# Kernel optimization log

Hardware: AMD Instinct MI355X
Metric: run time of the kernel (lower is better)

## Reference

```python
import jax, jax.numpy as jnp
import numpy as np

B, C, H, W = 32, 256, 64, 64
GROUPS = 32                      # factor
CG = C // GROUPS                 # channels per group = 8
EPS = 1e-5                       # GroupNorm eps (torch default)


def setup_inputs() -> dict:
    key = jax.random.key(0)
    ks = jax.random.split(key, 5)
    x = jax.random.normal(ks[0], (B, C, H, W), dtype=jnp.float32)
    # conv1x1: [out=CG, in=CG] (kernel 1x1 collapsed to a matrix)
    w1 = jax.random.normal(ks[1], (CG, CG), dtype=jnp.float32) * (1.0 / np.sqrt(CG))
    b1 = jax.random.normal(ks[2], (CG,), dtype=jnp.float32) * 0.01
    # conv3x3: OIHW [CG, CG, 3, 3]
    w3 = jax.random.normal(ks[3], (CG, CG, 3, 3), dtype=jnp.float32) * (1.0 / np.sqrt(9 * CG))
    b3 = jax.random.normal(ks[4], (CG,), dtype=jnp.float32) * 0.01
    # GroupNorm(num_groups=CG, num_channels=CG) affine params
    gn_w = jnp.ones((CG,), dtype=jnp.float32)
    gn_b = jnp.zeros((CG,), dtype=jnp.float32)
    return {"x": x, "w1": w1, "b1": b1, "w3": w3, "b3": b3, "gn_w": gn_w, "gn_b": gn_b}


def reference(x, w1, b1, w3, b3, gn_w, gn_b):
    b, c, h, w = x.shape
    cg = c // GROUPS
    bg = b * GROUPS
    gx = x.reshape(bg, cg, h, w)

    # coordinate pooling
    x_h = gx.mean(axis=3, keepdims=True)                       # [bg, cg, h, 1]
    x_w = gx.mean(axis=2, keepdims=True).transpose(0, 1, 3, 2)  # [bg, cg, w, 1]

    # conv1x1 over concatenated coordinates (pure channel mix)
    hw = jnp.einsum('oc,bclk->bolk', w1, jnp.concatenate([x_h, x_w], axis=2))
    hw = hw + b1[None, :, None, None]                           # [bg, cg, h+w, 1]
    xh = hw[:, :, :h, :]                                        # [bg, cg, h, 1]
    xw = hw[:, :, h:, :].transpose(0, 1, 3, 2)                  # [bg, cg, 1, w]

    gated = gx * jax.nn.sigmoid(xh) * jax.nn.sigmoid(xw)        # [bg, cg, h, w]

    # GroupNorm(num_groups=cg, num_channels=cg): per-(sample,channel) spatial norm
    mu = gated.mean(axis=(2, 3), keepdims=True)
    var = gated.var(axis=(2, 3), keepdims=True)                 # biased var, matches torch
    x1 = (gated - mu) * jax.lax.rsqrt(var + EPS)
    x1 = x1 * gn_w[None, :, None, None] + gn_b[None, :, None, None]

    # conv3x3, padding=1 (SAME)
    x2 = jax.lax.conv_general_dilated(
        gx, w3, window_strides=(1, 1), padding='SAME',
        dimension_numbers=('NCHW', 'OIHW', 'NCHW'))
    x2 = x2 + b3[None, :, None, None]                           # [bg, cg, h, w]

    # cross channel-attention: softmax over pooled channels, matmul with flattened maps
    x11 = jax.nn.softmax(x1.mean(axis=(2, 3)), axis=-1)         # [bg, cg]
    x21 = jax.nn.softmax(x2.mean(axis=(2, 3)), axis=-1)         # [bg, cg]
    x12 = x2.reshape(bg, cg, h * w)
    x22 = x1.reshape(bg, cg, h * w)
    y = jnp.einsum('bc,bcl->bl', x11, x12) + jnp.einsum('bc,bcl->bl', x21, x22)

    weights = jax.nn.sigmoid(y).reshape(bg, 1, h, w)
    return (gx * weights).reshape(b, c, h, w)
```

## Files before the change

kernel.cpp:

```cpp
#include <hip/hip_runtime.h>

#define EPS 1e-5f
#define PSTRIDE 1120

__launch_bounds__(256, 4)
__global__ void k1_stats(const float* __restrict__ x,
                         const float* __restrict__ w1,
                         const float* __restrict__ b1,
                         const float* __restrict__ w3,
                         const float* __restrict__ b3,
                         const float* __restrict__ gn_w,
                         const float* __restrict__ gn_b,
                         float* __restrict__ params)
{
  __shared__ float rs[512];
  __shared__ float cs[512];
  __shared__ float sh[512];
  __shared__ float sw[512];
  __shared__ float colpart[2048];
  __shared__ float wavepart[64];
  __shared__ float Ssum[8], mu_s[8], rstd_s[8], m2[8], x11[8], alpha[8];
  __shared__ float corners[32];
  __shared__ float kc_s;

  const int t    = threadIdx.x;
  const int g    = blockIdx.x;
  const int q    = t & 15;
  const int rg   = t >> 4;
  const int wv   = t >> 6;
  const int lane = t & 63;
  const float*  xg  = x + (size_t)g * 32768;
  const float4* xg4 = (const float4*)xg;

  float4 cacc[8];
#pragma unroll
  for (int c = 0; c < 8; ++c) cacc[c] = make_float4(0.f, 0.f, 0.f, 0.f);
#pragma unroll
  for (int c = 0; c < 8; ++c) {
#pragma unroll
    for (int k = 0; k < 4; ++k) {
      float4 v = xg4[c*1024 + t + 256*k];
      cacc[c].x += v.x; cacc[c].y += v.y; cacc[c].z += v.z; cacc[c].w += v.w;
      float rp = (v.x + v.y) + (v.z + v.w);
      rp += __shfl_xor(rp, 1, 64);
      rp += __shfl_xor(rp, 2, 64);
      rp += __shfl_xor(rp, 4, 64);
      rp += __shfl_xor(rp, 8, 64);
      if (q == 0) rs[c*64 + rg + 16*k] = rp;
    }
  }
#pragma unroll
  for (int c = 0; c < 8; ++c) {
    float sx = cacc[c].x, sy = cacc[c].y, sz = cacc[c].z, sww = cacc[c].w;
    sx += __shfl_xor(sx, 16, 64); sx += __shfl_xor(sx, 32, 64);
    sy += __shfl_xor(sy, 16, 64); sy += __shfl_xor(sy, 32, 64);
    sz += __shfl_xor(sz, 16, 64); sz += __shfl_xor(sz, 32, 64);
    sww += __shfl_xor(sww, 16, 64); sww += __shfl_xor(sww, 32, 64);
    if (lane < 16) *(float4*)&colpart[wv*512 + c*64 + lane*4] = make_float4(sx, sy, sz, sww);
  }
  __syncthreads();

#pragma unroll
  for (int r = 0; r < 2; ++r) {
    int idx = t + 256*r;
    cs[idx] = colpart[idx] + colpart[512 + idx] + colpart[1024 + idx] + colpart[1536 + idx];
  }
  if (t < 8) {
    float S = 0.f;
    for (int i = 0; i < 64; ++i) S += rs[t*64 + i];
    Ssum[t] = S;
  }
  if (t >= 32 && t < 64) {
    int ic = (t - 32) >> 2, cr = t & 3;
    int ofs = (cr == 0) ? 0 : (cr == 1) ? 63 : (cr == 2) ? 63*64 : 4095;
    corners[t - 32] = xg[ic*4096 + ofs];
  }
  __syncthreads();

#pragma unroll
  for (int r = 0; r < 2; ++r) {
    int idx = t + 256*r;
    int o = idx >> 6, i = idx & 63;
    float a1 = b1[o], a2 = a1;
#pragma unroll
    for (int c = 0; c < 8; ++c) {
      float wv1 = w1[o*8 + c];
      a1 = fmaf(wv1, rs[c*64 + i] * (1.f/64.f), a1);
      a2 = fmaf(wv1, cs[c*64 + i] * (1.f/64.f), a2);
    }
    sh[idx] = 1.f / (1.f + __expf(-a1));
    sw[idx] = 1.f / (1.f + __expf(-a2));
  }
  __syncthreads();

  float p1[8], p2[8];
#pragma unroll
  for (int c = 0; c < 8; ++c) { p1[c] = 0.f; p2[c] = 0.f; }
#pragma unroll
  for (int c = 0; c < 8; ++c) {
    const float4 sw4 = *(const float4*)&sw[c*64 + q*4];
#pragma unroll
    for (int k = 0; k < 4; ++k) {
      int i = rg + 16*k;
      float4 v = xg4[c*1024 + t + 256*k];
      float shv = sh[c*64 + i];
      float g0 = v.x*shv*sw4.x, g1 = v.y*shv*sw4.y;
      float g2 = v.z*shv*sw4.z, g3 = v.w*shv*sw4.w;
      p1[c] += (g0 + g1) + (g2 + g3);
      p2[c] += (g0*g0 + g1*g1) + (g2*g2 + g3*g3);
    }
  }
#pragma unroll
  for (int c = 0; c < 8; ++c) {
#pragma unroll
    for (int off = 1; off < 64; off <<= 1) {
      p1[c] += __shfl_xor(p1[c], off, 64);
      p2[c] += __shfl_xor(p2[c], off, 64);
    }
    if (lane == 0) { wavepart[wv*16 + c] = p1[c]; wavepart[wv*16 + 8 + c] = p2[c]; }
  }
  __syncthreads();

  if (t < 8) {
    float s1 = wavepart[t]     + wavepart[16 + t] + wavepart[32 + t] + wavepart[48 + t];
    float s2 = wavepart[8 + t] + wavepart[24 + t] + wavepart[40 + t] + wavepart[56 + t];
    float mu  = s1 * (1.f/4096.f);
    float var = s2 * (1.f/4096.f) - mu*mu;
    mu_s[t]   = mu;
    rstd_s[t] = rsqrtf(var + EPS);
  } else if (t >= 64 && t < 72) {
    int o = t - 64;
    float acc = 0.f;
    for (int ic = 0; ic < 8; ++ic) {
      float S   = Ssum[ic];
      float r0  = rs[ic*64 + 0],  r63 = rs[ic*64 + 63];
      float c0  = cs[ic*64 + 0],  c63 = cs[ic*64 + 63];
      float g00   = corners[ic*4 + 0];
      float g063  = corners[ic*4 + 1];
      float g630  = corners[ic*4 + 2];
      float g6363 = corners[ic*4 + 3];
      const float* w3p = w3 + (o*8 + ic)*9;
#pragma unroll
      for (int kh = 0; kh < 3; ++kh) {
        float rex = (kh == 0) ? r63 : (kh == 2) ? r0 : 0.f;
#pragma unroll
        for (int kw = 0; kw < 3; ++kw) {
          float cex = (kw == 0) ? c63 : (kw == 2) ? c0 : 0.f;
          float corner = 0.f;
          if      (kh == 0 && kw == 0) corner = g6363;
          else if (kh == 0 && kw == 2) corner = g630;
          else if (kh == 2 && kw == 0) corner = g063;
          else if (kh == 2 && kw == 2) corner = g00;
          acc = fmaf(w3p[kh*3 + kw], (S - rex - cex) + corner, acc);
        }
      }
    }
    m2[o] = b3[o] + acc * (1.f/4096.f);
  }
  __syncthreads();

  if (t == 0) {
    float e[8];
    float m = m2[0];
    for (int c = 1; c < 8; ++c) m = fmaxf(m, m2[c]);
    float ssum = 0.f;
    for (int c = 0; c < 8; ++c) { e[c] = __expf(m2[c] - m); ssum += e[c]; }
    float kc = 0.f;
    for (int c = 0; c < 8; ++c) {
      float x21 = e[c] / ssum;
      alpha[c] = x21 * gn_w[c] * rstd_s[c];
      kc += x21 * (gn_b[c] - gn_w[c] * rstd_s[c] * mu_s[c]);
    }
    float m1 = gn_b[0];
    for (int c = 1; c < 8; ++c) m1 = fmaxf(m1, gn_b[c]);
    float s1 = 0.f;
    for (int c = 0; c < 8; ++c) { e[c] = __expf(gn_b[c] - m1); s1 += e[c]; }
    for (int c = 0; c < 8; ++c) {
      float v = e[c] / s1;
      x11[c] = v;
      kc = fmaf(v, b3[c], kc);
    }
    kc_s = kc;
  }
  __syncthreads();

  float* P = params + (size_t)g * PSTRIDE;
#pragma unroll
  for (int r = 0; r < 2; ++r) {
    int idx = t + 256*r;
    int c = idx >> 6;
    P[idx]       = alpha[c] * sh[idx];
    P[512 + idx] = sw[idx];
  }
  if (t < 72) {
    float acc = 0.f;
#pragma unroll
    for (int o = 0; o < 8; ++o) acc = fmaf(x11[o], w3[o*72 + t], acc);
    P[1024 + t] = acc;
  }
  if (t == 128) P[1096] = kc_s;
}

__launch_bounds__(256, 4)
__global__ void k2_out(const float* __restrict__ x,
                       const float* __restrict__ params,
                       float* __restrict__ out)
{
  __shared__ float tile[8*18*64];
  __shared__ float pA[128];
  __shared__ float psw[512];
  __shared__ float pwf[72];
  __shared__ float pkc;

  const int t    = threadIdx.x;
  const int g    = blockIdx.x >> 2;
  const int tl   = blockIdx.x & 3;
  const int r0   = tl << 4;
  const int lane = t & 63;
  const float4* xg4 = (const float4*)(x + (size_t)g * 32768);
  float*        og  = out + (size_t)g * 32768;
  const float*  P   = params + (size_t)g * PSTRIDE;

#pragma unroll
  for (int k = 0; k < 9; ++k) {
    int f   = t + 256*k;
    int c   = f / 288;
    int rem = f - c*288;
    int r   = rem >> 4;
    int qq  = rem & 15;
    int row = r0 + r - 1;
    float4 v = make_float4(0.f, 0.f, 0.f, 0.f);
    if (row >= 0 && row <= 63) v = xg4[c*1024 + row*16 + qq];
    *(float4*)&tile[c*1152 + r*64 + (qq << 2)] = v;
  }
  if (t < 128) pA[t] = P[(t >> 4)*64 + r0 + (t & 15)];
#pragma unroll
  for (int r = 0; r < 2; ++r) { int idx = t + 256*r; psw[idx] = P[512 + idx]; }
  if (t < 72)  pwf[t] = P[1024 + t];
  if (t == 200) pkc = P[1096];
  __syncthreads();

  const int il = t >> 4;
  const int lx = t & 15;
  const int j4 = lx << 2;
  const int i  = r0 + il;

  float y0 = pkc, y1 = pkc, y2 = pkc, y3 = pkc;
#pragma unroll
  for (int ic = 0; ic < 8; ++ic) {
    const float* cb = &tile[ic*1152];
    float4 cen;
#pragma unroll
    for (int kh = 0; kh < 3; ++kh) {
      const float* rbase = cb + (il + kh)*64;
      float4 c4 = *(const float4*)(rbase + j4);
      float lv = __shfl_up(c4.w, 1, 64);
      float rv = __shfl_down(c4.x, 1, 64);
      if (lx == 0)  lv = 0.f;
      if (lx == 15) rv = 0.f;
      const float w0  = pwf[ic*9 + kh*3 + 0];
      const float w1v = pwf[ic*9 + kh*3 + 1];
      const float w2  = pwf[ic*9 + kh*3 + 2];
      y0 = fmaf(w0, lv,   fmaf(w1v, c4.x, fmaf(w2, c4.y, y0)));
      y1 = fmaf(w0, c4.x, fmaf(w1v, c4.y, fmaf(w2, c4.z, y1)));
      y2 = fmaf(w0, c4.y, fmaf(w1v, c4.z, fmaf(w2, c4.w, y2)));
      y3 = fmaf(w0, c4.z, fmaf(w1v, c4.w, fmaf(w2, rv,  y3)));
      if (kh == 1) cen = c4;
    }
    const float sg   = pA[ic*16 + il];
    const float4 sw4 = *(const float4*)&psw[ic*64 + j4];
    y0 = fmaf(sg * sw4.x, cen.x, y0);
    y1 = fmaf(sg * sw4.y, cen.y, y1);
    y2 = fmaf(sg * sw4.z, cen.z, y2);
    y3 = fmaf(sg * sw4.w, cen.w, y3);
  }
  const float wg0 = 1.f / (1.f + __expf(-y0));
  const float wg1 = 1.f / (1.f + __expf(-y1));
  const float wg2 = 1.f / (1.f + __expf(-y2));
  const float wg3 = 1.f / (1.f + __expf(-y3));
#pragma unroll
  for (int c = 0; c < 8; ++c) {
    const float4 cen = *(const float4*)&tile[c*1152 + (il + 1)*64 + j4];
    float4 o4;
    o4.x = cen.x * wg0;
    o4.y = cen.y * wg1;
    o4.z = cen.z * wg2;
    o4.w = cen.w * wg3;
    *(float4*)&og[c*4096 + i*64 + j4] = o4;
  }
}

extern "C" void kernel_launch(void* const* d_in, const int* in_sizes, int n_in,
                              void* d_out, int out_size, void* d_ws, size_t ws_size,
                              hipStream_t stream) {
  (void)in_sizes; (void)n_in; (void)out_size; (void)ws_size;
  const float* x    = (const float*)d_in[0];
  const float* w1   = (const float*)d_in[1];
  const float* b1   = (const float*)d_in[2];
  const float* w3   = (const float*)d_in[3];
  const float* b3   = (const float*)d_in[4];
  const float* gn_w = (const float*)d_in[5];
  const float* gn_b = (const float*)d_in[6];
  float* out    = (float*)d_out;
  float* params = (float*)d_ws;

  k1_stats<<<1024, 256, 0, stream>>>(x, w1, b1, w3, b3, gn_w, gn_b, params);
  k2_out  <<<4096, 256, 0, stream>>>(x, params, out);
}
```

Baseline: 339.1 us.

## Restructure stats kernel to one wave per channel with register-cached input

The stats kernel now launches 512 threads so each 64-lane wave owns one channel. Each wave loads its 4096-element channel once into 16 float4 registers and reuses them for row, column and total sums and for the gated variance pass, instead of reading x from global memory twice. Cross-wave shared-memory partial buffers and one barrier go away because each wave finishes its channel's reductions with shuffles alone. The cost is higher register pressure per thread, which may limit occupancy at 512 threads with launch bounds of 4 blocks.

```diff
diff --git a/kernel.cpp b/kernel.cpp
--- a/kernel.cpp
+++ b/kernel.cpp
@@ -3,7 +3,7 @@
 #define EPS 1e-5f
 #define PSTRIDE 1120
 
-__launch_bounds__(256, 4)
+__launch_bounds__(512, 4)
 __global__ void k1_stats(const float* __restrict__ x,
                          const float* __restrict__ w1,
                          const float* __restrict__ b1,
@@ -17,118 +17,96 @@
   __shared__ float cs[512];
   __shared__ float sh[512];
   __shared__ float sw[512];
-  __shared__ float colpart[2048];
-  __shared__ float wavepart[64];
   __shared__ float Ssum[8], mu_s[8], rstd_s[8], m2[8], x11[8], alpha[8];
   __shared__ float corners[32];
   __shared__ float kc_s;
 
-  const int t    = threadIdx.x;
-  const int g    = blockIdx.x;
-  const int q    = t & 15;
-  const int rg   = t >> 4;
-  const int wv   = t >> 6;
-  const int lane = t & 63;
-  const float*  xg  = x + (size_t)g * 32768;
-  const float4* xg4 = (const float4*)xg;
-
-  float4 cacc[8];
-#pragma unroll
-  for (int c = 0; c < 8; ++c) cacc[c] = make_float4(0.f, 0.f, 0.f, 0.f);
-#pragma unroll
-  for (int c = 0; c < 8; ++c) {
-#pragma unroll
-    for (int k = 0; k < 4; ++k) {
-      float4 v = xg4[c*1024 + t + 256*k];
-      cacc[c].x += v.x; cacc[c].y += v.y; cacc[c].z += v.z; cacc[c].w += v.w;
-      float rp = (v.x + v.y) + (v.z + v.w);
-      rp += __shfl_xor(rp, 1, 64);
-      rp += __shfl_xor(rp, 2, 64);
-      rp += __shfl_xor(rp, 4, 64);
-      rp += __shfl_xor(rp, 8, 64);
-      if (q == 0) rs[c*64 + rg + 16*k] = rp;
-    }
-  }
-#pragma unroll
-  for (int c = 0; c < 8; ++c) {
-    float sx = cacc[c].x, sy = cacc[c].y, sz = cacc[c].z, sww = cacc[c].w;
-    sx += __shfl_xor(sx, 16, 64); sx += __shfl_xor(sx, 32, 64);
-    sy += __shfl_xor(sy, 16, 64); sy += __shfl_xor(sy, 32, 64);
-    sz += __shfl_xor(sz, 16, 64); sz += __shfl_xor(sz, 32, 64);
-    sww += __shfl_xor(sww, 16, 64); sww += __shfl_xor(sww, 32, 64);
-    if (lane < 16) *(float4*)&colpart[wv*512 + c*64 + lane*4] = make_float4(sx, sy, sz, sww);
-  }
-  __syncthreads();
-
-#pragma unroll
-  for (int r = 0; r < 2; ++r) {
-    int idx = t + 256*r;
-    cs[idx] = colpart[idx] + colpart[512 + idx] + colpart[1024 + idx] + colpart[1536 + idx];
-  }
-  if (t < 8) {
-    float S = 0.f;
-    for (int i = 0; i < 64; ++i) S += rs[t*64 + i];
-    Ssum[t] = S;
-  }
-  if (t >= 32 && t < 64) {
-    int ic = (t - 32) >> 2, cr = t & 3;
-    int ofs = (cr == 0) ? 0 : (cr == 1) ? 63 : (cr == 2) ? 63*64 : 4095;
-    corners[t - 32] = xg[ic*4096 + ofs];
-  }
-  __syncthreads();
-
-#pragma unroll
-  for (int r = 0; r < 2; ++r) {
-    int idx = t + 256*r;
-    int o = idx >> 6, i = idx & 63;
-    float a1 = b1[o], a2 = a1;
+  const int t = threadIdx.x;
+  const int w = t >> 6;
+  const int l = t & 63;
+  const int s = l >> 4;
+  const int q = l & 15;
+  const int g = blockIdx.x;
+  const float4* xg4 = (const float4*)(x + (size_t)g * 32768);
+
+  float4 d[16];
+#pragma unroll
+  for (int k = 0; k < 16; ++k) d[k] = xg4[w*1024 + l + 64*k];
+
+#pragma unroll
+  for (int k = 0; k < 16; ++k) {
+    float rp = (d[k].x + d[k].y) + (d[k].z + d[k].w);
+    rp += __shfl_xor(rp, 1, 64);
+    rp += __shfl_xor(rp, 2, 64);
+    rp += __shfl_xor(rp, 4, 64);
+    rp += __shfl_xor(rp, 8, 64);
+    if (q == 0) rs[w*64 + s + 4*k] = rp;
+  }
+
+  float4 cacc = make_float4(0.f, 0.f, 0.f, 0.f);
+#pragma unroll
+  for (int k = 0; k < 16; ++k) {
+    cacc.x += d[k].x; cacc.y += d[k].y; cacc.z += d[k].z; cacc.w += d[k].w;
+  }
+  cacc.x += __shfl_xor(cacc.x, 16, 64); cacc.x += __shfl_xor(cacc.x, 32, 64);
+  cacc.y += __shfl_xor(cacc.y, 16, 64); cacc.y += __shfl_xor(cacc.y, 32, 64);
+  cacc.z += __shfl_xor(cacc.z, 16, 64); cacc.z += __shfl_xor(cacc.z, 32, 64);
+  cacc.w += __shfl_xor(cacc.w, 16, 64); cacc.w += __shfl_xor(cacc.w, 32, 64);
+  if (l < 16) *(float4*)&cs[w*64 + l*4] = cacc;
+
+  float tsum = (cacc.x + cacc.y) + (cacc.z + cacc.w);
+  tsum += __shfl_xor(tsum, 1, 64);
+  tsum += __shfl_xor(tsum, 2, 64);
+  tsum += __shfl_xor(tsum, 4, 64);
+  tsum += __shfl_xor(tsum, 8, 64);
+  if (l == 0) Ssum[w] = tsum;
+
+  if (l == 0)  corners[w*4 + 0] = d[0].x;
+  if (l == 15) corners[w*4 + 1] = d[0].w;
+  if (l == 48) corners[w*4 + 2] = d[15].x;
+  if (l == 63) corners[w*4 + 3] = d[15].w;
+  __syncthreads();
+
+  {
+    float a1 = b1[w], a2 = a1;
 #pragma unroll
     for (int c = 0; c < 8; ++c) {
-      float wv1 = w1[o*8 + c];
-      a1 = fmaf(wv1, rs[c*64 + i] * (1.f/64.f), a1);
-      a2 = fmaf(wv1, cs[c*64 + i] * (1.f/64.f), a2);
-    }
-    sh[idx] = 1.f / (1.f + __expf(-a1));
-    sw[idx] = 1.f / (1.f + __expf(-a2));
-  }
-  __syncthreads();
-
-  float p1[8], p2[8];
-#pragma unroll
-  for (int c = 0; c < 8; ++c) { p1[c] = 0.f; p2[c] = 0.f; }
-#pragma unroll
-  for (int c = 0; c < 8; ++c) {
-    const float4 sw4 = *(const float4*)&sw[c*64 + q*4];
-#pragma unroll
-    for (int k = 0; k < 4; ++k) {
-      int i = rg + 16*k;
-      float4 v = xg4[c*1024 + t + 256*k];
-      float shv = sh[c*64 + i];
-      float g0 = v.x*shv*sw4.x, g1 = v.y*shv*sw4.y;
-      float g2 = v.z*shv*sw4.z, g3 = v.w*shv*sw4.w;
-      p1[c] += (g0 + g1) + (g2 + g3);
-      p2[c] += (g0*g0 + g1*g1) + (g2*g2 + g3*g3);
-    }
-  }
-#pragma unroll
-  for (int c = 0; c < 8; ++c) {
+      float wv1 = w1[w*8 + c];
+      a1 = fmaf(wv1, rs[c*64 + l] * (1.f/64.f), a1);
+      a2 = fmaf(wv1, cs[c*64 + l] * (1.f/64.f), a2);
+    }
+    sh[t] = 1.f / (1.f + __expf(-a1));
+    sw[t] = 1.f / (1.f + __expf(-a2));
+  }
+  __syncthreads();
+
+  {
+    const float4 sw4 = *(const float4*)&sw[w*64 + q*4];
+    float p1 = 0.f, p2 = 0.f;
+#pragma unroll
+    for (int k = 0; k < 16; ++k) {
+      const float shv = sh[w*64 + s + 4*k];
+      float g0 = d[k].x * shv * sw4.x;
+      float g1 = d[k].y * shv * sw4.y;
+      float g2 = d[k].z * shv * sw4.z;
+      float g3 = d[k].w * shv * sw4.w;
+      p1 += (g0 + g1) + (g2 + g3);
+      p2 += (g0*g0 + g1*g1) + (g2*g2 + g3*g3);
+    }
 #pragma unroll
     for (int off = 1; off < 64; off <<= 1) {
-      p1[c] += __shfl_xor(p1[c], off, 64);
-      p2[c] += __shfl_xor(p2[c], off, 64);
-    }
-    if (lane == 0) { wavepart[wv*16 + c] = p1[c]; wavepart[wv*16 + 8 + c] = p2[c]; }
-  }
-  __syncthreads();
-
-  if (t < 8) {
-    float s1 = wavepart[t]     + wavepart[16 + t] + wavepart[32 + t] + wavepart[48 + t];
-    float s2 = wavepart[8 + t] + wavepart[24 + t] + wavepart[40 + t] + wavepart[56 + t];
-    float mu  = s1 * (1.f/4096.f);
-    float var = s2 * (1.f/4096.f) - mu*mu;
-    mu_s[t]   = mu;
-    rstd_s[t] = rsqrtf(var + EPS);
-  } else if (t >= 64 && t < 72) {
+      p1 += __shfl_xor(p1, off, 64);
+      p2 += __shfl_xor(p2, off, 64);
+    }
+    if (l == 0) {
+      float mu  = p1 * (1.f/4096.f);
+      float var = p2 * (1.f/4096.f) - mu*mu;
+      mu_s[w]   = mu;
+      rstd_s[w] = rsqrtf(var + EPS);
+    }
+  }
+
+  if (t >= 64 && t < 72) {
     int o = t - 64;
     float acc = 0.f;
     for (int ic = 0; ic < 8; ++ic) {
@@ -185,13 +163,8 @@
   __syncthreads();
 
   float* P = params + (size_t)g * PSTRIDE;
-#pragma unroll
-  for (int r = 0; r < 2; ++r) {
-    int idx = t + 256*r;
-    int c = idx >> 6;
-    P[idx]       = alpha[c] * sh[idx];
-    P[512 + idx] = sw[idx];
-  }
+  P[t]       = alpha[w] * sh[t];
+  P[512 + t] = sw[t];
   if (t < 72) {
     float acc = 0.f;
 #pragma unroll
@@ -216,7 +189,6 @@
   const int g    = blockIdx.x >> 2;
   const int tl   = blockIdx.x & 3;
   const int r0   = tl << 4;
-  const int lane = t & 63;
   const float4* xg4 = (const float4*)(x + (size_t)g * 32768);
   float*        og  = out + (size_t)g * 32768;
   const float*  P   = params + (size_t)g * PSTRIDE;
@@ -304,6 +276,6 @@
   float* out    = (float*)d_out;
   float* params = (float*)d_ws;
 
-  k1_stats<<<1024, 256, 0, stream>>>(x, w1, b1, w3, b3, gn_w, gn_b, params);
+  k1_stats<<<1024, 512, 0, stream>>>(x, w1, b1, w3, b3, gn_w, gn_b, params);
   k2_out  <<<4096, 256, 0, stream>>>(x, params, out);
 }
```

Result: faster. 285.9 us (-15.7%).
